# Kernel tuning notes

Hardware: AMD Instinct MI355X
Metric: run time of the kernel (lower is better)

Reference implementation:

```python
import jax, jax.numpy as jnp
import numpy as np

B, N, FEAT, BB, LD = 512, 50, 300, 300, 2048
D1 = BB + FEAT        # 600 = s_with_bb dim
D2 = 2 * D1           # 1200 = combined dim


def _fc(x, w, b):
    # ReLUWithWeightNormFC: weight-norm is a reparametrization of a plain
    # linear, so math-equivalently ReLU(x @ W^T + b).
    return jax.nn.relu(x @ w.T + b)


def setup_inputs() -> dict:
    key = jax.random.key(0)
    ks = jax.random.split(key, 32)

    def p(k, shape):
        return jax.random.normal(k, shape, dtype=jnp.float32) * 0.02

    inp = {
        "l": jax.random.normal(ks[0], (B, LD), dtype=jnp.float32),
        "s": jax.random.normal(ks[1], (B, N, FEAT), dtype=jnp.float32),
        "ps": jax.random.uniform(ks[2], (B, N, 4), dtype=jnp.float32),
        "mask_s": jax.random.randint(ks[3], (B,), 0, 50, dtype=jnp.int32),
        "bb_w": p(ks[4], (BB, 10)),       "bb_b": p(ks[5], (BB,)),
        "fa1_w": p(ks[6], (D1, D1)),      "fa1_b": p(ks[7], (D1,)),
        "fa2_w": p(ks[8], (D1, D1)),      "fa2_b": p(ks[9], (D1,)),
        "fa3_w": p(ks[10], (D2, D2)),     "fa3_b": p(ks[11], (D2,)),
        "fa4_w": p(ks[12], (D2, D2)),     "fa4_b": p(ks[13], (D2,)),
        "fa5_w": p(ks[14], (D2, D2)),     "fa5_b": p(ks[15], (D2,)),
        "lp1_w": p(ks[16], (D2, LD)),     "lp1_b": p(ks[17], (D2,)),
        "lp2_w": p(ks[18], (D2, LD)),     "lp2_b": p(ks[19], (D2,)),
        "out_w": p(ks[20], (FEAT, D2)),   "out_b": p(ks[21], (FEAT,)),
    }
    return inp


def reference(l, s, ps, mask_s,
              bb_w, bb_b, fa1_w, fa1_b, fa2_w, fa2_b, fa3_w, fa3_b,
              fa4_w, fa4_b, fa5_w, fa5_b, lp1_w, lp1_b, lp2_w, lp2_b,
              out_w, out_b):
    # ---- bb_process ----
    size = ps[..., 2:] - ps[..., :2]                       # [B,N,2]
    centre = ps[..., :2] + 0.5 * size                      # [B,N,2]
    area = (size[..., 0] * size[..., 1])[..., None]        # [B,N,1]
    shape = (size[..., 0] / (size[..., 1] + 1e-14))[..., None]
    bb_in = jnp.concatenate([ps, size, centre, area, shape], axis=-1)  # [B,N,10]
    bb = _fc(bb_in, bb_w, bb_b)                            # [B,N,BB]

    s_bb = jnp.concatenate([s, bb], axis=-1)               # [B,N,D1]

    # ---- masked adjacency bias (order of assignments preserved) ----
    i = jnp.arange(N)
    mx = jnp.maximum(i[None, :], i[:, None])               # [N,N]
    m1 = mx[None, :, :] < mask_s[:, None, None]            # [B,N,N]
    m2 = i[None, :, None] >= mask_s[:, None, None]         # row index >= mask_s
    inf_tmp = jnp.where(m1 | m2, 0.0, -jnp.inf)
    inf_tmp = jnp.where(jnp.eye(N, dtype=bool)[None], -jnp.inf, inf_tmp)
    inf_tmp = inf_tmp.at[:, 0, 0].set(
        jnp.where(mask_s == 1, 0.0, inf_tmp[:, 0, 0]))

    # l projections are identical across the 50 nodes -> compute once, broadcast
    lp1 = _fc(l, lp1_w, lp1_b)[:, None, :]                 # [B,1,D2]
    lp2 = _fc(l, lp2_w, lp2_b)[:, None, :]                 # [B,1,D2]

    # ---- one GNN iteration (it=1) ----
    combined = jnp.concatenate(
        [s_bb, _fc(s_bb, fa1_w, fa1_b) * _fc(s_bb, fa2_w, fa2_b)], axis=-1)  # [B,N,D2]
    l_masked_source = _fc(combined, fa3_w, fa3_b) * lp1    # [B,N,D2]
    adj = jnp.einsum('bnd,bmd->bnm', _fc(combined, fa4_w, fa4_b),
                     l_masked_source)                      # [B,N,N]
    adj = jax.nn.softmax(adj + inf_tmp, axis=2)
    prepared = _fc(combined, fa5_w, fa5_b) * lp2           # [B,N,D2]
    messages = _fc(jnp.einsum('bnm,bmd->bnd', adj, prepared), out_w, out_b)
    s_out = jnp.concatenate([s, messages], axis=-1)        # [B,N,2*FEAT]

    output_mask = (i[None, :] < mask_s[:, None])[:, :, None]  # [B,N,1]
    return s_out * output_mask.astype(s_out.dtype), adj
```

## Files before the change

### kernel.cpp

```cpp
#include <hip/hip_runtime.h>
#include <stdint.h>

typedef unsigned short u16;
typedef unsigned int u32;
typedef __attribute__((ext_vector_type(8))) __bf16 bf16x8;
typedef __attribute__((ext_vector_type(4))) float f32x4;

#define DEVINL static __device__ __forceinline__

DEVINL u16 f2bf(float x) {
  u32 u = __float_as_uint(x);
  return (u16)((u + (((u >> 16) & 1u) + 0x7fffu)) >> 16);
}
DEVINL float bf2f(u16 h) { return __uint_as_float(((u32)h) << 16); }

DEVINL void async16(const void* g, void* l) {
  void* g2 = const_cast<void*>(g);
  __builtin_amdgcn_global_load_lds((__attribute__((address_space(1))) void*)g2,
                                   (__attribute__((address_space(3))) void*)l,
                                   16, 0, 0);
}

DEVINL void swz_xy(int& bx, int& by) {
  const int gx = (int)gridDim.x;
  const int nwg = gx * (int)gridDim.y;
  const int bid = (int)blockIdx.y * gx + (int)blockIdx.x;
  const int q = nwg >> 3, r = nwg & 7, x = bid & 7, t = bid >> 3;
  const int s = (x < r ? x * (q + 1) : r * (q + 1) + (x - r) * q) + t;
  bx = s % gx;
  by = s / gx;
}


__global__ void k_pack_w(const float* src, int n, int k, u16* hi, u16* lo,
                         int KP, long total, int gap) {
  long i = (long)blockIdx.x * 256 + threadIdx.x;
  if (i >= total) return;
  int r = (int)(i / KP);
  int c = (int)(i - (long)r * KP);
  int sc = c;
  bool ok = (r < n);
  if (gap) {
    if (c >= 600 && c < 640) ok = false;
    else if (c >= 640) sc = c - 40;
  }
  if (sc >= k) ok = false;
  float x = ok ? src[(size_t)r * k + sc] : 0.f;
  u16 h = f2bf(x);
  hi[i] = h;
  if (lo) lo[i] = f2bf(x - bf2f(h));
}

__global__ void k_pack_bias(const float* src, int n, float* dst, int NP) {
  int i = blockIdx.x * 256 + threadIdx.x;
  if (i < NP) dst[i] = (i < n) ? src[i] : 0.f;
}

__global__ void k_bb(const float* s_c, const float* ps_c, const float* bb_w,
                     const float* bb_b, const int* mask_s, u16* Chi, u16* Clo,
                     float* outp, int r0) {
  int rn = blockIdx.x;
  int grow = r0 + rn;
  int b = grow / 50;
  int n = grow - b * 50;
  float keep = (n < mask_s[b]) ? 1.f : 0.f;
  const float* p = ps_c + (size_t)rn * 4;
  float p0 = p[0], p1 = p[1], p2 = p[2], p3 = p[3];
  float sz0 = p2 - p0, sz1 = p3 - p1;
  float bin[10];
  bin[0] = p0; bin[1] = p1; bin[2] = p2; bin[3] = p3;
  bin[4] = sz0; bin[5] = sz1;
  bin[6] = p0 + 0.5f * sz0; bin[7] = p1 + 0.5f * sz1;
  bin[8] = sz0 * sz1; bin[9] = sz0 / (sz1 + 1e-14f);
  for (int c = threadIdx.x; c < 640; c += 256) {
    float x = 0.f;
    if (c < 300) {
      x = s_c[(size_t)rn * 300 + c];
      outp[(size_t)grow * 600 + c] = keep * x;
    } else if (c < 600) {
      int j = c - 300;
      float a = bb_b[j];
      const float* wr = bb_w + j * 10;
#pragma unroll
      for (int kk = 0; kk < 10; ++kk) a += bin[kk] * wr[kk];
      x = fmaxf(a, 0.f);
    }
    u16 h = f2bf(x);
    Chi[(size_t)rn * 1280 + c] = h;
    Clo[(size_t)rn * 1280 + c] = f2bf(x - bf2f(h));
  }
}


DEVINL void gemm_fused3(const u16* Ahp, const u16* Alp, const u16* Bhp,
                        const u16* Blp, int lda, int ldw, int ksteps,
                        u16* S, f32x4 (&acc)[4][4]) {
  const int tid = threadIdx.x;
  const int lane = tid & 63;
  const int wv = tid >> 6;
  const int wr = (wv >> 1) * 64;
  const int wc = (wv & 1) * 64;
  const int mrow = lane & 15;
  const int q = lane >> 4;

  const int c0 = tid, c1 = tid + 256;
  const int p0 = ((c0 & 3) ^ ((c0 >> 3) & 3)) * 8;
  const int p1 = ((c1 & 3) ^ ((c1 >> 3) & 3)) * 8;
  const long ao0 = (long)(c0 >> 2) * lda + p0;
  const long ao1 = (long)(c1 >> 2) * lda + p1;
  const long bo0 = (long)(c0 >> 2) * ldw + p0;
  const long bo1 = (long)(c1 >> 2) * ldw + p1;

  int aoffs[4], boffs[4];
#pragma unroll
  for (int k = 0; k < 4; ++k) {
    const int ra = wr + mrow + 16 * k;
    const int rb = wc + mrow + 16 * k;
    aoffs[k] = ra * 32 + ((q ^ ((ra >> 1) & 3)) << 3);
    boffs[k] = rb * 32 + ((q ^ ((rb >> 1) & 3)) << 3);
  }

  auto issueF = [&](int ph) {
    const long ta = (long)(ph >> 1) * 32;
    const u16* sa = (ph & 1) ? Alp : Ahp;
    const u16* sb = (ph & 1) ? Blp : Bhp;
    u16* d = S + (ph & 3) * 8192;
    async16(sa + ta + ao0, d + c0 * 8);
    async16(sa + ta + ao1, d + c1 * 8);
    async16(sb + ta + bo0, d + 4096 + c0 * 8);
    async16(sb + ta + bo1, d + 4096 + c1 * 8);
  };

  const int total = 2 * ksteps;
  issueF(0); issueF(1); if (total > 2) issueF(2);
  bf16x8 ah[4], bh[4];
  for (int i = 0; i < ksteps; ++i) {
    {
      const int rem = total - 1 - 2 * i;
      if (rem >= 2)      asm volatile("s_waitcnt vmcnt(8)" ::: "memory");
      else               asm volatile("s_waitcnt vmcnt(4)" ::: "memory");
      __builtin_amdgcn_sched_barrier(0);
      __builtin_amdgcn_s_barrier();
      __builtin_amdgcn_sched_barrier(0);
      if (2 * i + 3 < total) issueF(2 * i + 3);
      const u16* hb = S + ((2 * i) & 3) * 8192;
#pragma unroll
      for (int k = 0; k < 4; ++k) {
        ah[k] = *(const bf16x8*)(hb + aoffs[k]);
        bh[k] = *(const bf16x8*)(hb + 4096 + boffs[k]);
      }
#pragma unroll
      for (int mi = 0; mi < 4; ++mi)
#pragma unroll
        for (int nj = 0; nj < 4; ++nj)
          acc[mi][nj] = __builtin_amdgcn_mfma_f32_16x16x32_bf16(
              ah[mi], bh[nj], acc[mi][nj], 0, 0, 0);
    }
    {
      const int rem = total - 2 - 2 * i;
      if (rem >= 2)      asm volatile("s_waitcnt vmcnt(8)" ::: "memory");
      else if (rem == 1) asm volatile("s_waitcnt vmcnt(4)" ::: "memory");
      else               asm volatile("s_waitcnt vmcnt(0)" ::: "memory");
      __builtin_amdgcn_sched_barrier(0);
      __builtin_amdgcn_s_barrier();
      __builtin_amdgcn_sched_barrier(0);
      if (2 * i + 4 < total) issueF(2 * i + 4);
      const u16* hb = S + ((2 * i + 1) & 3) * 8192;
      bf16x8 al[4], bl[4];
#pragma unroll
      for (int k = 0; k < 4; ++k) {
        al[k] = *(const bf16x8*)(hb + aoffs[k]);
        bl[k] = *(const bf16x8*)(hb + 4096 + boffs[k]);
      }
#pragma unroll
      for (int mi = 0; mi < 4; ++mi)
#pragma unroll
        for (int nj = 0; nj < 4; ++nj)
          acc[mi][nj] = __builtin_amdgcn_mfma_f32_16x16x32_bf16(
              al[mi], bh[nj], acc[mi][nj], 0, 0, 0);
#pragma unroll
      for (int mi = 0; mi < 4; ++mi)
#pragma unroll
        for (int nj = 0; nj < 4; ++nj)
          acc[mi][nj] = __builtin_amdgcn_mfma_f32_16x16x32_bf16(
              ah[mi], bl[nj], acc[mi][nj], 0, 0, 0);
    }
  }
}

DEVINL void gemm_core1(const u16* Ab, const u16* Bb, int lda, int ldw,
                       int ksteps, u16* As, u16* Bs, f32x4 (&acc)[4][4]) {
  const int tid = threadIdx.x;
  const int lane = tid & 63;
  const int wv = tid >> 6;
  const int wr = (wv >> 1) * 64;
  const int wc = (wv & 1) * 64;
  const int mrow = lane & 15;
  const int q = lane >> 4;

  const int c0 = tid, c1 = tid + 256;
  const int p0 = ((c0 & 3) ^ ((c0 >> 3) & 3)) * 8;
  const int p1 = ((c1 & 3) ^ ((c1 >> 3) & 3)) * 8;
  const long ao0 = (long)(c0 >> 2) * lda + p0;
  const long ao1 = (long)(c1 >> 2) * lda + p1;
  const long bo0 = (long)(c0 >> 2) * ldw + p0;
  const long bo1 = (long)(c1 >> 2) * ldw + p1;

  int aoffs[4], boffs[4];
#pragma unroll
  for (int k = 0; k < 4; ++k) {
    const int ra = wr + mrow + 16 * k;
    const int rb = wc + mrow + 16 * k;
    aoffs[k] = ra * 32 + ((q ^ ((ra >> 1) & 3)) << 3);
    boffs[k] = rb * 32 + ((q ^ ((rb >> 1) & 3)) << 3);
  }

  auto issue = [&](int sl, int t) {
    const long ta = (long)t * 32;
    u16* dA = As + sl * 4096;
    u16* dB = Bs + sl * 4096;
    async16(Ab + ta + ao0, dA + c0 * 8);
    async16(Ab + ta + ao1, dA + c1 * 8);
    async16(Bb + ta + bo0, dB + c0 * 8);
    async16(Bb + ta + bo1, dB + c1 * 8);
  };

  const int npro = ksteps < 3 ? ksteps : 3;
  for (int j = 0; j < npro; ++j) issue(j, j);
  int cs = 0, is = 3;
  for (int i = 0; i < ksteps; ++i) {
    const int rem = ksteps - 1 - i;
    if (rem >= 2)      asm volatile("s_waitcnt vmcnt(8)" ::: "memory");
    else if (rem == 1) asm volatile("s_waitcnt vmcnt(4)" ::: "memory");
    else               asm volatile("s_waitcnt vmcnt(0)" ::: "memory");
    __builtin_amdgcn_sched_barrier(0);
    __builtin_amdgcn_s_barrier();
    __builtin_amdgcn_sched_barrier(0);
    if (i + 3 < ksteps) { issue(is, i + 3); is = (is + 1) & 3; }
    const u16* Sa = As + cs * 4096;
    const u16* Sb = Bs + cs * 4096;
    cs = (cs + 1) & 3;
    bf16x8 af[4], bv[4];
#pragma unroll
    for (int k = 0; k < 4; ++k) af[k] = *(const bf16x8*)(Sa + aoffs[k]);
#pragma unroll
    for (int k = 0; k < 4; ++k) bv[k] = *(const bf16x8*)(Sb + boffs[k]);
#pragma unroll
    for (int mi = 0; mi < 4; ++mi)
#pragma unroll
      for (int nj = 0; nj < 4; ++nj)
        acc[mi][nj] = __builtin_amdgcn_mfma_f32_16x16x32_bf16(
            af[mi], bv[nj], acc[mi][nj], 0, 0, 0);
  }
}

DEVINL void gemm_core2(const u16* const Aph[3], const u16* const B1ph[3],
                       const u16* const B2ph[3], int lda, int ldw, int ksteps,
                       u16* As, u16* B1s, u16* B2s, f32x4 (&a1)[4][4],
                       f32x4 (&a2)[4][4]) {
  const int tid = threadIdx.x;
  const int lane = tid & 63;
  const int wv = tid >> 6;
  const int wr = (wv >> 1) * 64;
  const int wc = (wv & 1) * 64;
  const int mrow = lane & 15;
  const int q = lane >> 4;

  const int c0 = tid, c1 = tid + 256;
  const int p0 = ((c0 & 3) ^ ((c0 >> 3) & 3)) * 8;
  const int p1 = ((c1 & 3) ^ ((c1 >> 3) & 3)) * 8;
  const long ao0 = (long)(c0 >> 2) * lda + p0;
  const long ao1 = (long)(c1 >> 2) * lda + p1;
  const long bo0 = (long)(c0 >> 2) * ldw + p0;
  const long bo1 = (long)(c1 >> 2) * ldw + p1;

  int aoffs[4], boffs[4];
#pragma unroll
  for (int k = 0; k < 4; ++k) {
    const int ra = wr + mrow + 16 * k;
    const int rb = wc + mrow + 16 * k;
    aoffs[k] = ra * 32 + ((q ^ ((ra >> 1) & 3)) << 3);
    boffs[k] = rb * 32 + ((q ^ ((rb >> 1) & 3)) << 3);
  }

  const u16* Aa1 = Aph[1]; const u16* Ba1 = B1ph[1]; const u16* Ca1 = B2ph[1];
  const u16* Aa2 = Aph[2]; const u16* Ba2 = B1ph[2]; const u16* Ca2 = B2ph[2];
  const u16* An = Aph[0];  const u16* Bn = B1ph[0];  const u16* Cn = B2ph[0];
  int tn = 0, pn = 0;
  const int total = 3 * ksteps;

  auto issue = [&](int sl) {
    const u16* ga = An + (long)tn * 32;
    const u16* g1 = Bn + (long)tn * 32;
    const u16* g2 = Cn + (long)tn * 32;
    u16* dA = As + sl * 4096;
    u16* d1 = B1s + sl * 4096;
    u16* d2 = B2s + sl * 4096;
    async16(ga + ao0, dA + c0 * 8);
    async16(ga + ao1, dA + c1 * 8);
    async16(g1 + bo0, d1 + c0 * 8);
    async16(g1 + bo1, d1 + c1 * 8);
    async16(g2 + bo0, d2 + c0 * 8);
    async16(g2 + bo1, d2 + c1 * 8);
    if (++tn == ksteps) {
      tn = 0; ++pn;
      if (pn == 1) { An = Aa1; Bn = Ba1; Cn = Ca1; }
      else if (pn == 2) { An = Aa2; Bn = Ba2; Cn = Ca2; }
    }
  };

  issue(0);
  issue(1);
  int slot = 0;
  for (int i = 0; i < total; ++i) {
    if (i + 1 < total) asm volatile("s_waitcnt vmcnt(6)" ::: "memory");
    else               asm volatile("s_waitcnt vmcnt(0)" ::: "memory");
    __builtin_amdgcn_sched_barrier(0);
    __builtin_amdgcn_s_barrier();
    __builtin_amdgcn_sched_barrier(0);
    if (i + 2 < total) {
      int s2 = slot + 2; if (s2 >= 3) s2 -= 3;
      issue(s2);
    }
    const u16* Sa = As + slot * 4096;
    const u16* S1 = B1s + slot * 4096;
    const u16* S2 = B2s + slot * 4096;
    bf16x8 af[4], b1v[4], b2v[4];
#pragma unroll
    for (int k = 0; k < 4; ++k) af[k] = *(const bf16x8*)(Sa + aoffs[k]);
#pragma unroll
    for (int k = 0; k < 4; ++k) b1v[k] = *(const bf16x8*)(S1 + boffs[k]);
#pragma unroll
    for (int k = 0; k < 4; ++k) b2v[k] = *(const bf16x8*)(S2 + boffs[k]);
#pragma unroll
    for (int mi = 0; mi < 4; ++mi)
#pragma unroll
      for (int nj = 0; nj < 4; ++nj)
        a1[mi][nj] = __builtin_amdgcn_mfma_f32_16x16x32_bf16(
            af[mi], b1v[nj], a1[mi][nj], 0, 0, 0);
#pragma unroll
    for (int mi = 0; mi < 4; ++mi)
#pragma unroll
      for (int nj = 0; nj < 4; ++nj)
        a2[mi][nj] = __builtin_amdgcn_mfma_f32_16x16x32_bf16(
            af[mi], b2v[nj], a2[mi][nj], 0, 0, 0);
    if (++slot == 3) slot = 0;
  }
}

#define GEMM_EPI_IDX                                                    \
  const int lane = threadIdx.x & 63, wv = threadIdx.x >> 6;             \
  const int wr = (wv >> 1) * 64, wc = (wv & 1) * 64;                    \
  const int mcol = lane & 15, q = lane >> 4;                            \
  const int gm0 = by * 128, gn0 = bx * 128;

__global__ __launch_bounds__(256) void k_gemm_fa12(const u16* Ah, const u16* Al,
    const u16* W1h, const u16* W1l, const u16* W2h, const u16* W2l,
    const float* bias, u16* Chi, u16* Clo) {
  __shared__ __align__(16) u16 As[12288], B1s[12288], B2s[12288];
  int bx, by; swz_xy(bx, by);
  const size_t arow = (size_t)by * 128 * 1280;
  const size_t wrow = (size_t)bx * 128 * 640;
  const u16* Aph[3]  = {Ah + arow, Al + arow, Ah + arow};
  const u16* B1ph[3] = {W1h + wrow, W1h + wrow, W1l + wrow};
  const u16* B2ph[3] = {W2h + wrow, W2h + wrow, W2l + wrow};
  f32x4 a1[4][4] = {}, a2[4][4] = {};
  gemm_core2(Aph, B1ph, B2ph, 1280, 640, 20, As, B1s, B2s, a1, a2);
  GEMM_EPI_IDX
#pragma unroll
  for (int mi = 0; mi < 4; ++mi)
#pragma unroll
    for (int r = 0; r < 4; ++r) {
      int grow = gm0 + wr + mi * 16 + q * 4 + r;
#pragma unroll
      for (int ni = 0; ni < 4; ++ni) {
        int gcol = gn0 + wc + ni * 16 + mcol;
        float v1 = fmaxf(a1[mi][ni][r] + bias[gcol], 0.f);
        float v2 = fmaxf(a2[mi][ni][r] + bias[640 + gcol], 0.f);
        float y = v1 * v2;
        u16 h = f2bf(y);
        Chi[(size_t)grow * 1280 + 640 + gcol] = h;
        Clo[(size_t)grow * 1280 + 640 + gcol] = f2bf(y - bf2f(h));
      }
    }
}

__global__ __launch_bounds__(256) void k_gemm_lp(const u16* Ah, const u16* Al,
    const u16* Wh, const u16* Wl, const float* bias, float* outp) {
  __shared__ __align__(16) u16 S[32768];
  int bx, by; swz_xy(bx, by);
  const size_t arow = (size_t)by * 128 * 2048;
  const size_t wrow = (size_t)bx * 128 * 2048;
  f32x4 acc[4][4] = {};
  gemm_fused3(Ah + arow, Al + arow, Wh + wrow, Wl + wrow, 2048, 2048, 64, S,
              acc);
  GEMM_EPI_IDX
#pragma unroll
  for (int mi = 0; mi < 4; ++mi)
#pragma unroll
    for (int r = 0; r < 4; ++r) {
      int grow = gm0 + wr + mi * 16 + q * 4 + r;
#pragma unroll
      for (int ni = 0; ni < 4; ++ni) {
        int gcol = gn0 + wc + ni * 16 + mcol;
        outp[(size_t)grow * 2560 + gcol] = fmaxf(acc[mi][ni][r] + bias[gcol], 0.f);
      }
    }
}

__global__ __launch_bounds__(256) void k_gemm_fa345(const u16* Ah, const u16* Al,
    const u16* Wh, const u16* Wl, const u16* W5h, const float* b34,
    const float* b5, const float* lp_o, u16* fa3h, u16* fa3l, u16* fa4h,
    u16* fa4l, u16* fa5o, int r0) {
  __shared__ __align__(16) u16 S[32768];
  int bx, by; swz_xy(bx, by);
  const size_t arow = (size_t)by * 128 * 1280;
  const int gn0 = bx * 128;
  f32x4 acc[4][4] = {};
  if (gn0 < 2560) {
    const size_t wrow = (size_t)gn0 * 1280;
    gemm_fused3(Ah + arow, Al + arow, Wh + wrow, Wl + wrow, 1280, 1280, 40, S,
                acc);
  } else {
    const size_t wrow = (size_t)(gn0 - 2560) * 1280;
    gemm_core1(Ah + arow, W5h + wrow, 1280, 1280, 40, S, S + 16384, acc);
  }
  const int lane = threadIdx.x & 63, wv = threadIdx.x >> 6;
  const int wr = (wv >> 1) * 64, wc = (wv & 1) * 64;
  const int mcol = lane & 15, q = lane >> 4;
  const int gm0 = by * 128;
  if (gn0 < 2560) {
    const int seg = (gn0 >= 1280);
    u16* dsth = seg ? fa4h : fa3h;
    u16* dstl = seg ? fa4l : fa3l;
#pragma unroll
    for (int mi = 0; mi < 4; ++mi)
#pragma unroll
      for (int r = 0; r < 4; ++r) {
        int grow = gm0 + wr + mi * 16 + q * 4 + r;
        int b = (r0 + grow) / 50;
        const float* lpb = lp_o + (size_t)b * 2560;
#pragma unroll
        for (int ni = 0; ni < 4; ++ni) {
          int gcol = gn0 + wc + ni * 16 + mcol;
          int c = seg ? gcol - 1280 : gcol;
          float v = fmaxf(acc[mi][ni][r] + b34[gcol], 0.f);
          if (!seg) v *= lpb[c];
          if (c < 1216) {
            u16 h = f2bf(v);
            dsth[(size_t)grow * 1216 + c] = h;
            dstl[(size_t)grow * 1216 + c] = f2bf(v - bf2f(h));
          }
        }
      }
  } else {
#pragma unroll
    for (int mi = 0; mi < 4; ++mi)
#pragma unroll
      for (int r = 0; r < 4; ++r) {
        int grow = gm0 + wr + mi * 16 + q * 4 + r;
        int b = (r0 + grow) / 50;
        const float* lpb = lp_o + (size_t)b * 2560 + 1280;
#pragma unroll
        for (int ni = 0; ni < 4; ++ni) {
          int gcol = (gn0 - 2560) + wc + ni * 16 + mcol;
          float v = fmaxf(acc[mi][ni][r] + b5[gcol], 0.f) * lpb[gcol];
          if (gcol < 1216) fa5o[(size_t)grow * 1216 + gcol] = f2bf(v);
        }
      }
  }
}

__global__ __launch_bounds__(256) void k_gemm_out(const u16* A, const u16* Wh,
    const float* bias, const int* mask_s, float* outp, int r0) {
  __shared__ __align__(16) u16 S[32768];
  int bx, by; swz_xy(bx, by);
  const size_t arow = (size_t)by * 128 * 1216;
  const size_t wrow = (size_t)bx * 128 * 1216;
  f32x4 acc[4][4] = {};
  gemm_core1(A + arow, Wh + wrow, 1216, 1216, 38, S, S + 16384, acc);
  GEMM_EPI_IDX
#pragma unroll
  for (int mi = 0; mi < 4; ++mi)
#pragma unroll
    for (int r = 0; r < 4; ++r) {
      int grow = r0 + gm0 + wr + mi * 16 + q * 4 + r;
      int b = grow / 50;
      int n = grow - b * 50;
      float keep = (n < mask_s[b]) ? 1.f : 0.f;
#pragma unroll
      for (int ni = 0; ni < 4; ++ni) {
        int gcol = gn0 + wc + ni * 16 + mcol;
        float v = fmaxf(acc[mi][ni][r] + bias[gcol], 0.f) * keep;
        if (gcol < 300) outp[(size_t)grow * 600 + 300 + gcol] = v;
      }
    }
}

__global__ __launch_bounds__(256) void k_attn(const u16* fa3h, const u16* fa3l,
    const u16* fa4h, const u16* fa4l, const u16* fa5o, const int* mask_s,
    float* adj_out, u16* msg, int b0) {
  __shared__ __align__(16) u16 stg[32768];
  __shared__ float Ssc[64 * 64];
  const int bl = blockIdx.x;
  const int bg = b0 + bl;
  const int tid = threadIdx.x, lane = tid & 63, wv = tid >> 6;
  const int mrow = lane & 15, q = lane >> 4;
  const size_t base = (size_t)bl * 50 * 1216;

  {
    const int srow = tid >> 2;
    const int srcRow = srow < 50 ? srow : 49;
    const size_t gsoff = base + (size_t)srcRow * 1216 +
                         (size_t)(((tid & 3) ^ ((tid >> 3) & 3)) * 8);
    auto issueP1 = [&](int sl, int s) {
      const int p = (s >= 76) ? 2 : (s >= 38 ? 1 : 0);
      const int t = s - p * 38;
      const u16* Ap = (p == 1) ? fa4l : fa4h;
      const u16* Bp = (p == 2) ? fa3l : fa3h;
      u16* d = stg + sl * 4096;
      async16(Ap + gsoff + (size_t)t * 32, d + tid * 8);
      async16(Bp + gsoff + (size_t)t * 32, d + 2048 + tid * 8);
    };
    const int ra = wv * 16 + mrow;
    const int aoff = ra * 32 + ((q ^ ((ra >> 1) & 3)) << 3);
    int boff[4];
#pragma unroll
    for (int ni = 0; ni < 4; ++ni) {
      const int rb = ni * 16 + mrow;
      boff[ni] = rb * 32 + ((q ^ ((rb >> 1) & 3)) << 3);
    }
    for (int j = 0; j < 7; ++j) issueP1(j, j);
    f32x4 acc[4] = {};
    int cs = 0, is = 7;
    for (int i = 0; i < 114; ++i) {
      const int rem = 113 - i;
      if (rem >= 6)      asm volatile("s_waitcnt vmcnt(12)" ::: "memory");
      else if (rem == 5) asm volatile("s_waitcnt vmcnt(10)" ::: "memory");
      else if (rem == 4) asm volatile("s_waitcnt vmcnt(8)" ::: "memory");
      else if (rem == 3) asm volatile("s_waitcnt vmcnt(6)" ::: "memory");
      else if (rem == 2) asm volatile("s_waitcnt vmcnt(4)" ::: "memory");
      else if (rem == 1) asm volatile("s_waitcnt vmcnt(2)" ::: "memory");
      else               asm volatile("s_waitcnt vmcnt(0)" ::: "memory");
      __builtin_amdgcn_sched_barrier(0);
      __builtin_amdgcn_s_barrier();
      __builtin_amdgcn_sched_barrier(0);
      if (i + 7 < 114) { issueP1(is, i + 7); if (++is == 8) is = 0; }
      const u16* d = stg + cs * 4096;
      if (++cs == 8) cs = 0;
      bf16x8 af = *(const bf16x8*)(d + aoff);
#pragma unroll
      for (int ni = 0; ni < 4; ++ni) {
        bf16x8 bv = *(const bf16x8*)(d + 2048 + boff[ni]);
        acc[ni] =
            __builtin_amdgcn_mfma_f32_16x16x32_bf16(af, bv, acc[ni], 0, 0, 0);
      }
    }
#pragma unroll
    for (int ni = 0; ni < 4; ++ni)
#pragma unroll
      for (int r = 0; r < 4; ++r)
        Ssc[(wv * 16 + q * 4 + r) * 64 + ni * 16 + mrow] = acc[ni][r];
  }
  __syncthreads();

  const int c0 = tid, c1 = tid + 256;
  const int m0 = c0 >> 3, d0 = (c0 & 7) * 8;
  const int m1 = c1 >> 3, d1 = (c1 & 7) * 8;
  const size_t g0 = base + (size_t)(m0 < 50 ? m0 : 49) * 1216 + d0;
  const size_t g1 = base + (size_t)(m1 < 50 ? m1 : 49) * 1216 + d1;
  auto issueP3 = [&](int sl, int s) {
    u16* d = stg + sl * 4096;
    async16(fa5o + g0 + (size_t)s * 64, d + c0 * 8);
    async16(fa5o + g1 + (size_t)s * 64, d + c1 * 8);
  };
  for (int j = 0; j < 7; ++j) issueP3(j, j);

  {
    const int mk = mask_s[bg];
    for (int n = wv; n < 50; n += 4) {
      int mm = lane;
      float v = -__builtin_inff();
      if (mm < 50) {
        int mx2 = n > mm ? n : mm;
        bool valid = (mx2 < mk) || (n >= mk);
        if (mm == n) valid = false;
        if (n == 0 && mm == 0 && mk == 1) valid = true;
        if (valid) v = Ssc[n * 64 + mm];
      }
      float mx = v;
      for (int o = 32; o > 0; o >>= 1) mx = fmaxf(mx, __shfl_down(mx, o));
      mx = __shfl(mx, 0);
      float e = __expf(v - mx);
      float sm = e;
      for (int o = 32; o > 0; o >>= 1) sm += __shfl_down(sm, o);
      sm = __shfl(sm, 0);
      float pv = e / sm;
      if (mm < 50) {
        adj_out[((size_t)bg * 50 + n) * 50 + mm] = pv;
        Ssc[n * 64 + mm] = pv;
      } else {
        Ssc[n * 64 + mm] = 0.f;
      }
    }
  }
  __syncthreads();

  {
    int cs = 0, is = 7;
    for (int dt = 0; dt < 19; ++dt) {
      const int rem = 18 - dt;
      if (rem >= 6)      asm volatile("s_waitcnt vmcnt(12)" ::: "memory");
      else if (rem == 5) asm volatile("s_waitcnt vmcnt(10)" ::: "memory");
      else if (rem == 4) asm volatile("s_waitcnt vmcnt(8)" ::: "memory");
      else if (rem == 3) asm volatile("s_waitcnt vmcnt(6)" ::: "memory");
      else if (rem == 2) asm volatile("s_waitcnt vmcnt(4)" ::: "memory");
      else if (rem == 1) asm volatile("s_waitcnt vmcnt(2)" ::: "memory");
      else               asm volatile("s_waitcnt vmcnt(0)" ::: "memory");
      __builtin_amdgcn_sched_barrier(0);
      __builtin_amdgcn_s_barrier();
      __builtin_amdgcn_sched_barrier(0);
      if (dt + 7 < 19) { issueP3(is, dt + 7); if (++is == 8) is = 0; }
      const u16* d = stg + cs * 4096;
      if (++cs == 8) cs = 0;
      f32x4 a3[4] = {};
#pragma unroll
      for (int ks = 0; ks < 2; ++ks) {
        bf16x8 af;
#pragma unroll
        for (int j = 0; j < 8; ++j)
          af[j] = (__bf16)Ssc[(wv * 16 + mrow) * 64 + ks * 32 + q * 8 + j];
#pragma unroll
        for (int ni = 0; ni < 4; ++ni) {
          bf16x8 bv;
#pragma unroll
          for (int j = 0; j < 8; ++j)
            bv[j] = *(const __bf16*)(d + (ks * 32 + q * 8 + j) * 64 + ni * 16 + mrow);
          a3[ni] = __builtin_amdgcn_mfma_f32_16x16x32_bf16(af, bv, a3[ni], 0, 0, 0);
        }
      }
#pragma unroll
      for (int ni = 0; ni < 4; ++ni)
#pragma unroll
        for (int r = 0; r < 4; ++r) {
          int n = wv * 16 + q * 4 + r;
          if (n < 50)
            msg[((size_t)bl * 50 + n) * 1216 + dt * 64 + ni * 16 + mrow] =
                f2bf(a3[ni][r]);
        }
    }
  }
}

extern "C" void kernel_launch(void* const* d_in, const int* in_sizes, int n_in,
                              void* d_out_, int out_size, void* d_ws,
                              size_t ws_size, hipStream_t stream) {
  (void)in_sizes; (void)n_in; (void)out_size;
  const float* l_in = (const float*)d_in[0];
  const float* s_in = (const float*)d_in[1];
  const float* ps   = (const float*)d_in[2];
  const int*   msk  = (const int*)d_in[3];
  const float* bbw  = (const float*)d_in[4];
  const float* bbb  = (const float*)d_in[5];
  const float* fa1w = (const float*)d_in[6];
  const float* fa1b = (const float*)d_in[7];
  const float* fa2w = (const float*)d_in[8];
  const float* fa2b = (const float*)d_in[9];
  const float* fa3w = (const float*)d_in[10];
  const float* fa3b = (const float*)d_in[11];
  const float* fa4w = (const float*)d_in[12];
  const float* fa4b = (const float*)d_in[13];
  const float* fa5w = (const float*)d_in[14];
  const float* fa5b = (const float*)d_in[15];
  const float* lp1w = (const float*)d_in[16];
  const float* lp1b = (const float*)d_in[17];
  const float* lp2w = (const float*)d_in[18];
  const float* lp2b = (const float*)d_in[19];
  const float* outw = (const float*)d_in[20];
  const float* outb = (const float*)d_in[21];
  float* outp = (float*)d_out_;

  char* wsb = (char*)d_ws;
  size_t off = 0;
  auto alloc = [&](size_t bytes) -> char* {
    char* p = wsb + off;
    off = (off + bytes + 255) & ~(size_t)255;
    return p;
  };
  u16*   l_hi   = (u16*)alloc(512ull * 2048 * 2);
  u16*   l_lo   = (u16*)alloc(512ull * 2048 * 2);
  u16*   Wout   = (u16*)alloc(384ull * 1216 * 2);
  float* b_fa12 = (float*)alloc(1280 * 4);
  float* b_fa34 = (float*)alloc(2560 * 4);
  float* b_fa5  = (float*)alloc(1280 * 4);
  float* b_lp   = (float*)alloc(2560 * 4);
  float* b_out  = (float*)alloc(384 * 4);
  float* lp_o   = (float*)alloc(512ull * 2560 * 4);
  u16*   slab   = (u16*)alloc(10485760ull * 2);
  u16* Wlph   = slab;
  u16* Wlpl   = slab + 5242880;
  u16* Wfa1h  = slab;
  u16* Wfa1l  = slab + 409600;
  u16* Wfa2h  = slab + 819200;
  u16* Wfa2l  = slab + 1228800;
  u16* Wfa34h = slab + 1638400;
  u16* Wfa34l = slab + 4915200;
  u16* Wfa5h  = slab + 8192000;

  size_t ws_eff = ws_size ? ws_size : (size_t)512 * 1024 * 1024;
  long RN = 3200;
  const long opts[4] = {25600, 12800, 6400, 3200};
  for (int i = 0; i < 4; ++i) {
    size_t need = off + (size_t)17280 * opts[i] + 8 * 256;
    if (need <= ws_eff) { RN = opts[i]; break; }
  }
  u16*  Chi  = (u16*)alloc((size_t)RN * 1280 * 2);
  u16*  Clo  = (u16*)alloc((size_t)RN * 1280 * 2);
  u16*  fa5o = (u16*)alloc((size_t)RN * 1216 * 2);
  u16*  fa3h = (u16*)alloc((size_t)RN * 1216 * 2);
  u16*  fa3l = (u16*)alloc((size_t)RN * 1216 * 2);
  u16*  fa4h = (u16*)alloc((size_t)RN * 1216 * 2);
  u16*  fa4l = (u16*)alloc((size_t)RN * 1216 * 2);
  u16*  msg  = Chi;
  float* adj_o = outp + 15360000;

  dim3 T(256);
  k_pack_bias<<<dim3(3), T, 0, stream>>>(fa1b, 600, b_fa12, 640);
  k_pack_bias<<<dim3(3), T, 0, stream>>>(fa2b, 600, b_fa12 + 640, 640);
  k_pack_bias<<<dim3(5), T, 0, stream>>>(fa3b, 1200, b_fa34, 1280);
  k_pack_bias<<<dim3(5), T, 0, stream>>>(fa4b, 1200, b_fa34 + 1280, 1280);
  k_pack_bias<<<dim3(5), T, 0, stream>>>(fa5b, 1200, b_fa5, 1280);
  k_pack_bias<<<dim3(5), T, 0, stream>>>(lp1b, 1200, b_lp, 1280);
  k_pack_bias<<<dim3(5), T, 0, stream>>>(lp2b, 1200, b_lp + 1280, 1280);
  k_pack_bias<<<dim3(2), T, 0, stream>>>(outb, 300, b_out, 384);

  auto packw = [&](const float* src, int n, int k, u16* hi, u16* lo, int KP,
                   long total, int gap) {
    k_pack_w<<<dim3((unsigned)((total + 255) / 256)), T, 0, stream>>>(
        src, n, k, hi, lo, KP, total, gap);
  };
  packw(l_in, 512, 2048, l_hi, l_lo, 2048, 512L * 2048, 0);
  packw(outw, 300, 1200, Wout, nullptr, 1216, 384L * 1216, 0);

  packw(lp1w, 1200, 2048, Wlph, Wlpl, 2048, 1280L * 2048, 0);
  packw(lp2w, 1200, 2048, Wlph + 1280 * 2048, Wlpl + 1280 * 2048, 2048,
        1280L * 2048, 0);
  k_gemm_lp<<<dim3(20, 4), T, 0, stream>>>(l_hi, l_lo, Wlph, Wlpl, b_lp, lp_o);

  packw(fa1w, 600, 600, Wfa1h, Wfa1l, 640, 640L * 640, 0);
  packw(fa2w, 600, 600, Wfa2h, Wfa2l, 640, 640L * 640, 0);
  packw(fa3w, 1200, 1200, Wfa34h, Wfa34l, 1280, 1280L * 1280, 1);
  packw(fa4w, 1200, 1200, Wfa34h + 1638400, Wfa34l + 1638400, 1280,
        1280L * 1280, 1);
  packw(fa5w, 1200, 1200, Wfa5h, nullptr, 1280, 1280L * 1280, 1);

  const int nch = (int)(25600 / RN);
  const unsigned gy = (unsigned)(RN / 128);
  for (int c = 0; c < nch; ++c) {
    const int r0 = (int)(c * RN);
    const int b0 = r0 / 50;
    k_bb<<<dim3((unsigned)RN), T, 0, stream>>>(s_in + (size_t)r0 * 300,
                                               ps + (size_t)r0 * 4, bbw, bbb,
                                               msk, Chi, Clo, outp, r0);
    k_gemm_fa12<<<dim3(5, gy), T, 0, stream>>>(Chi, Clo, Wfa1h, Wfa1l, Wfa2h,
                                               Wfa2l, b_fa12, Chi, Clo);
    k_gemm_fa345<<<dim3(30, gy), T, 0, stream>>>(Chi, Clo, Wfa34h, Wfa34l,
                                                 Wfa5h, b_fa34, b_fa5, lp_o,
                                                 fa3h, fa3l, fa4h, fa4l, fa5o,
                                                 r0);
    k_attn<<<dim3((unsigned)(RN / 50)), T, 0, stream>>>(fa3h, fa3l, fa4h, fa4l,
                                                        fa5o, msk, adj_o, msg,
                                                        b0);
    k_gemm_out<<<dim3(3, gy), T, 0, stream>>>(msg, Wout, b_out, msk, outp, r0);
  }
}
```

Before: 1.465 ms.

## Split fa345 GEMM into 256x256-tile 8-wave fa34 kernel and separate fa5 kernel

Replaces the combined fa3/fa4/fa5 GEMM with two kernels. The fa3/fa4 part, which uses a split-bf16 three-MFMA scheme, now runs in a 512-thread kernel with 256x256 tiles. It double-buffers LDS through async global-to-LDS loads and raises wave priority around the MFMAs. The fa5 part becomes its own single-precision-pass kernel, and the minimum chunk size rises from 3200 to 6400 rows so RN stays divisible by 256. The larger tiles are meant to increase operand reuse and cut LDS/global traffic, at the cost of higher register and LDS pressure and an extra launch.

Result: faster. 1.401 ms (-4.4%).

```diff
diff --git a/kernel.cpp b/kernel.cpp
--- a/kernel.cpp
+++ b/kernel.cpp
@@ -408,67 +408,145 @@
     }
 }
 
-__global__ __launch_bounds__(256) void k_gemm_fa345(const u16* Ah, const u16* Al,
-    const u16* Wh, const u16* Wl, const u16* W5h, const float* b34,
-    const float* b5, const float* lp_o, u16* fa3h, u16* fa3l, u16* fa4h,
-    u16* fa4l, u16* fa5o, int r0) {
+__global__ __launch_bounds__(512, 2) void k_gemm_fa34(const u16* Ah,
+    const u16* Al, const u16* Wh, const u16* Wl, const float* b34,
+    const float* lp_o, u16* fa3h, u16* fa3l, u16* fa4h, u16* fa4l, int r0) {
+  __shared__ __align__(16) u16 S[2][4][8192];
+  int bx, by; swz_xy(bx, by);
+  const int tid = threadIdx.x;
+  const int lane = tid & 63, wv = tid >> 6;
+  const int wm = wv >> 2, wn = wv & 3;
+  const int mrow = lane & 15, q = lane >> 4;
+
+  const size_t arow = (size_t)by * 256 * 1280;
+  const size_t wrow = (size_t)bx * 256 * 1280;
+  const u16* mats[4] = {Ah + arow, Al + arow, Wh + wrow, Wl + wrow};
+
+  long soff[2];
+#pragma unroll
+  for (int j = 0; j < 2; ++j) {
+    const int c = j * 512 + tid;
+    soff[j] = (long)(c >> 2) * 1280 + ((c & 3) ^ ((c >> 3) & 3)) * 8;
+  }
+  int aoffs[8], boffs[4];
+#pragma unroll
+  for (int k = 0; k < 8; ++k) {
+    const int r = wm * 128 + k * 16 + mrow;
+    aoffs[k] = r * 32 + ((q ^ ((r >> 1) & 3)) << 3);
+  }
+#pragma unroll
+  for (int k = 0; k < 4; ++k) {
+    const int r = wn * 64 + k * 16 + mrow;
+    boffs[k] = r * 32 + ((q ^ ((r >> 1) & 3)) << 3);
+  }
+
+  f32x4 acc[8][4] = {};
+  const int ks = 40;
+
+#pragma unroll
+  for (int m = 0; m < 4; ++m) {
+    async16(mats[m] + soff[0], &S[0][m][tid * 8]);
+    async16(mats[m] + soff[1], &S[0][m][(512 + tid) * 8]);
+  }
+  asm volatile("s_waitcnt vmcnt(0)" ::: "memory");
+  __builtin_amdgcn_sched_barrier(0);
+  __builtin_amdgcn_s_barrier();
+
+  for (int t = 0; t < ks; ++t) {
+    const int cur = t & 1;
+    const long ta = (long)(t + 1) * 32;
+    const bool more = (t + 1 < ks);
+    bf16x8 bh[4], bl[4];
+#pragma unroll
+    for (int p = 0; p < 8; ++p) {
+      if (p == 0) {
+#pragma unroll
+        for (int k = 0; k < 4; ++k) {
+          bh[k] = *(const bf16x8*)(&S[cur][2][0] + boffs[k]);
+          bl[k] = *(const bf16x8*)(&S[cur][3][0] + boffs[k]);
+        }
+      }
+      bf16x8 ah = *(const bf16x8*)(&S[cur][0][0] + aoffs[p]);
+      bf16x8 al = *(const bf16x8*)(&S[cur][1][0] + aoffs[p]);
+      if (p < 4 && more) {
+        async16(mats[p] + ta + soff[0], &S[cur ^ 1][p][tid * 8]);
+        async16(mats[p] + ta + soff[1], &S[cur ^ 1][p][(512 + tid) * 8]);
+      }
+      __builtin_amdgcn_s_barrier();
+      asm volatile("s_waitcnt lgkmcnt(0)" ::: "memory");
+      __builtin_amdgcn_sched_barrier(0);
+      __builtin_amdgcn_s_setprio(1);
+#pragma unroll
+      for (int j = 0; j < 4; ++j)
+        acc[p][j] = __builtin_amdgcn_mfma_f32_16x16x32_bf16(ah, bh[j],
+                                                            acc[p][j], 0, 0, 0);
+#pragma unroll
+      for (int j = 0; j < 4; ++j)
+        acc[p][j] = __builtin_amdgcn_mfma_f32_16x16x32_bf16(al, bh[j],
+                                                            acc[p][j], 0, 0, 0);
+#pragma unroll
+      for (int j = 0; j < 4; ++j)
+        acc[p][j] = __builtin_amdgcn_mfma_f32_16x16x32_bf16(ah, bl[j],
+                                                            acc[p][j], 0, 0, 0);
+      __builtin_amdgcn_s_setprio(0);
+      __builtin_amdgcn_s_barrier();
+    }
+    if (more) {
+      asm volatile("s_waitcnt vmcnt(0)" ::: "memory");
+      __builtin_amdgcn_sched_barrier(0);
+      __builtin_amdgcn_s_barrier();
+    }
+  }
+
+  const int gm0 = by * 256, gn0 = bx * 256;
+  const int seg = (gn0 >= 1280);
+  u16* dsth = seg ? fa4h : fa3h;
+  u16* dstl = seg ? fa4l : fa3l;
+#pragma unroll
+  for (int p = 0; p < 8; ++p)
+#pragma unroll
+    for (int r = 0; r < 4; ++r) {
+      const int grow = gm0 + wm * 128 + p * 16 + q * 4 + r;
+      const int b = (r0 + grow) / 50;
+      const float* lpb = lp_o + (size_t)b * 2560;
+#pragma unroll
+      for (int j = 0; j < 4; ++j) {
+        const int gcol = gn0 + wn * 64 + j * 16 + mrow;
+        const int c = gcol - seg * 1280;
+        float v = fmaxf(acc[p][j][r] + b34[gcol], 0.f);
+        if (!seg) v *= lpb[c];
+        if (c < 1216) {
+          u16 h = f2bf(v);
+          dsth[(size_t)grow * 1216 + c] = h;
+          dstl[(size_t)grow * 1216 + c] = f2bf(v - bf2f(h));
+        }
+      }
+    }
+}
+
+__global__ __launch_bounds__(256) void k_gemm_fa5(const u16* Ah,
+    const u16* W5h, const float* b5, const float* lp_o, u16* fa5o, int r0) {
   __shared__ __align__(16) u16 S[32768];
   int bx, by; swz_xy(bx, by);
   const size_t arow = (size_t)by * 128 * 1280;
-  const int gn0 = bx * 128;
+  const size_t wrow = (size_t)bx * 128 * 1280;
   f32x4 acc[4][4] = {};
-  if (gn0 < 2560) {
-    const size_t wrow = (size_t)gn0 * 1280;
-    gemm_fused3(Ah + arow, Al + arow, Wh + wrow, Wl + wrow, 1280, 1280, 40, S,
-                acc);
-  } else {
-    const size_t wrow = (size_t)(gn0 - 2560) * 1280;
-    gemm_core1(Ah + arow, W5h + wrow, 1280, 1280, 40, S, S + 16384, acc);
-  }
-  const int lane = threadIdx.x & 63, wv = threadIdx.x >> 6;
-  const int wr = (wv >> 1) * 64, wc = (wv & 1) * 64;
-  const int mcol = lane & 15, q = lane >> 4;
-  const int gm0 = by * 128;
-  if (gn0 < 2560) {
-    const int seg = (gn0 >= 1280);
-    u16* dsth = seg ? fa4h : fa3h;
-    u16* dstl = seg ? fa4l : fa3l;
-#pragma unroll
-    for (int mi = 0; mi < 4; ++mi)
-#pragma unroll
-      for (int r = 0; r < 4; ++r) {
-        int grow = gm0 + wr + mi * 16 + q * 4 + r;
-        int b = (r0 + grow) / 50;
-        const float* lpb = lp_o + (size_t)b * 2560;
-#pragma unroll
-        for (int ni = 0; ni < 4; ++ni) {
-          int gcol = gn0 + wc + ni * 16 + mcol;
-          int c = seg ? gcol - 1280 : gcol;
-          float v = fmaxf(acc[mi][ni][r] + b34[gcol], 0.f);
-          if (!seg) v *= lpb[c];
-          if (c < 1216) {
-            u16 h = f2bf(v);
-            dsth[(size_t)grow * 1216 + c] = h;
-            dstl[(size_t)grow * 1216 + c] = f2bf(v - bf2f(h));
-          }
-        }
-      }
-  } else {
-#pragma unroll
-    for (int mi = 0; mi < 4; ++mi)
-#pragma unroll
-      for (int r = 0; r < 4; ++r) {
-        int grow = gm0 + wr + mi * 16 + q * 4 + r;
-        int b = (r0 + grow) / 50;
-        const float* lpb = lp_o + (size_t)b * 2560 + 1280;
-#pragma unroll
-        for (int ni = 0; ni < 4; ++ni) {
-          int gcol = (gn0 - 2560) + wc + ni * 16 + mcol;
-          float v = fmaxf(acc[mi][ni][r] + b5[gcol], 0.f) * lpb[gcol];
-          if (gcol < 1216) fa5o[(size_t)grow * 1216 + gcol] = f2bf(v);
-        }
-      }
-  }
+  gemm_core1(Ah + arow, W5h + wrow, 1280, 1280, 40, S, S + 16384, acc);
+  GEMM_EPI_IDX
+#pragma unroll
+  for (int mi = 0; mi < 4; ++mi)
+#pragma unroll
+    for (int r = 0; r < 4; ++r) {
+      int grow = gm0 + wr + mi * 16 + q * 4 + r;
+      int b = (r0 + grow) / 50;
+      const float* lpb = lp_o + (size_t)b * 2560 + 1280;
+#pragma unroll
+      for (int ni = 0; ni < 4; ++ni) {
+        int gcol = gn0 + wc + ni * 16 + mcol;
+        float v = fmaxf(acc[mi][ni][r] + b5[gcol], 0.f) * lpb[gcol];
+        if (gcol < 1216) fa5o[(size_t)grow * 1216 + gcol] = f2bf(v);
+      }
+    }
 }
 
 __global__ __launch_bounds__(256) void k_gemm_out(const u16* A, const u16* Wh,
@@ -708,9 +786,9 @@
   u16* Wfa5h  = slab + 8192000;
 
   size_t ws_eff = ws_size ? ws_size : (size_t)512 * 1024 * 1024;
-  long RN = 3200;
-  const long opts[4] = {25600, 12800, 6400, 3200};
-  for (int i = 0; i < 4; ++i) {
+  long RN = 6400;
+  const long opts[3] = {25600, 12800, 6400};
+  for (int i = 0; i < 3; ++i) {
     size_t need = off + (size_t)17280 * opts[i] + 8 * 256;
     if (need <= ws_eff) { RN = opts[i]; break; }
   }
@@ -764,10 +842,10 @@
                                                msk, Chi, Clo, outp, r0);
     k_gemm_fa12<<<dim3(5, gy), T, 0, stream>>>(Chi, Clo, Wfa1h, Wfa1l, Wfa2h,
                                                Wfa2l, b_fa12, Chi, Clo);
-    k_gemm_fa345<<<dim3(30, gy), T, 0, stream>>>(Chi, Clo, Wfa34h, Wfa34l,
-                                                 Wfa5h, b_fa34, b_fa5, lp_o,
-                                                 fa3h, fa3l, fa4h, fa4l, fa5o,
-                                                 r0);
+    k_gemm_fa34<<<dim3(10, (unsigned)(RN / 256)), dim3(512), 0, stream>>>(
+        Chi, Clo, Wfa34h, Wfa34l, b_fa34, lp_o, fa3h, fa3l, fa4h, fa4l, r0);
+    k_gemm_fa5<<<dim3(10, gy), T, 0, stream>>>(Chi, Wfa5h, b_fa5, lp_o, fa5o,
+                                               r0);
     k_attn<<<dim3((unsigned)(RN / 50)), T, 0, stream>>>(fa3h, fa3l, fa4h, fa4l,
                                                         fa5o, msk, adj_o, msg,
                                                         b0);
```
